# Kernel tuning notes

Measured on AMD Instinct MI355X. Metric: run time of the kernel, lower is better.

## Reference

```python
import jax, jax.numpy as jnp
import numpy as np
import math

L = 8           # n_layers
DIM = 1024
H = 16          # num_heads
HD = DIM // H   # head_dim
HID = 4096      # mlp hidden
V = 32000       # vocab
B, T = 2, 1024


def setup_inputs() -> dict:
    key = jax.random.key(0)
    ks = jax.random.split(key, 10)
    s = 0.02
    inp = {
        "input_ids": jax.random.randint(ks[0], (B, T), 0, V, dtype=jnp.int32),
        "labels": jax.random.randint(ks[1], (B, T), 0, V, dtype=jnp.int32),
        "Wemb": jax.random.normal(ks[2], (V, DIM), jnp.float32) * s,   # tied embed / lm_head
        "Wq": jax.random.normal(ks[3], (L, DIM, DIM), jnp.float32) * s,
        "Wk": jax.random.normal(ks[4], (L, DIM, DIM), jnp.float32) * s,
        "Wv": jax.random.normal(ks[5], (L, DIM, DIM), jnp.float32) * s,
        "Wo": jax.random.normal(ks[6], (L, DIM, DIM), jnp.float32) * s,
        "Wfc": jax.random.normal(ks[7], (L, DIM, HID), jnp.float32) * s,
        "Wgate": jax.random.normal(ks[8], (L, DIM, HID), jnp.float32) * s,
        "Wproj": jax.random.normal(ks[9], (L, HID, DIM), jnp.float32) * s,
    }
    return inp


def _forward(input_ids, labels, Wemb, Wq, Wk, Wv, Wo, Wfc, Wgate, Wproj):
    b, t = input_ids.shape
    h = Wemb[input_ids]                                   # [B,T,C] embedding lookup
    # causal additive mask: -inf strictly above diagonal
    mask = jnp.triu(jnp.full((t, t), -jnp.inf, dtype=h.dtype), k=1)
    inv_sqrt_L = 1.0 / math.sqrt(L)
    inv_sqrt_hd = 1.0 / math.sqrt(HD)
    inv_sqrt_hid = 1.0 / math.sqrt(HID)

    def block(h, params):
        wq, wk, wv, wo, wfc, wgate, wproj = params
        # attention (explicit QK^T softmax V, as in source)
        q = (h @ wq).reshape(b, t, H, HD)
        k = (h @ wk).reshape(b, t, H, HD)
        v = (h @ wv).reshape(b, t, H, HD)
        scores = jnp.einsum("bqhd,bkhd->bhqk", q, k) * inv_sqrt_hd + mask
        probs = jax.nn.softmax(scores, axis=-1)
        attn = jnp.einsum("bhqk,bkhd->bqhd", probs, v).reshape(b, t, DIM)
        h = h + (attn @ wo) * inv_sqrt_L
        # SwiGLU MLP with 1/sqrt(hidden) scaling
        mlp = (((h @ wfc) * jax.nn.silu(h @ wgate)) * inv_sqrt_hid) @ wproj
        h = h + mlp * inv_sqrt_L
        return h, None

    h, _ = jax.lax.scan(block, h, (Wq, Wk, Wv, Wo, Wfc, Wgate, Wproj))

    logits = h @ Wemb.T                                   # tied lm_head [B,T,V]
    # cross entropy with ignore_index=-1
    lab = labels.reshape(-1)
    valid = lab != -1
    safe = jnp.where(valid, lab, 0)
    logp = jax.nn.log_softmax(logits.reshape(-1, V), axis=-1)
    nll = -jnp.take_along_axis(logp, safe[:, None], axis=-1)[:, 0]
    loss = jnp.sum(jnp.where(valid, nll, 0.0)) / jnp.maximum(jnp.sum(valid), 1)
    return logits, loss


def reference(input_ids, labels, Wemb, Wq, Wk, Wv, Wo, Wfc, Wgate, Wproj):
    return _forward(input_ids, labels, Wemb, Wq, Wk, Wv, Wo, Wfc, Wgate, Wproj)
```

## Files before the change

### kernel.cpp

```cpp
#include <hip/hip_runtime.h>
#include <hip/hip_bf16.h>
#include <math.h>

#define L_LAYERS 8
#define DIM 1024
#define NH 16
#define HD 64
#define HID 4096
#define VOCAB 32000
#define BB 2
#define TT 1024
#define MROWS (BB*TT)

typedef unsigned short u16;
typedef short short8 __attribute__((ext_vector_type(8)));
typedef float f32x4 __attribute__((ext_vector_type(4)));
typedef unsigned short us4 __attribute__((ext_vector_type(4)));
typedef unsigned short us8 __attribute__((ext_vector_type(8)));

__device__ __forceinline__ float bf2f(u16 x){
  union { unsigned int u; float f; } v; v.u = ((unsigned int)x) << 16; return v.f;
}
__device__ __forceinline__ u16 f2bf(float f){
  union { float f; unsigned int u; } v; v.f = f;
  unsigned int r = (v.u + 0x7fffu + ((v.u >> 16) & 1u)) >> 16; return (u16)r;
}

#define AS1 __attribute__((address_space(1)))
#define AS3 __attribute__((address_space(3)))
__device__ __forceinline__ void gld_lds16(const void* g, void* l){
  __builtin_amdgcn_global_load_lds((const AS1 void*)g, (AS3 void*)l, 16, 0, 0);
}

__global__ void k_embed(const int* __restrict__ ids, const float* __restrict__ Wemb,
                        float* __restrict__ h, u16* __restrict__ hb){
  int bt = blockIdx.x; long id = ids[bt];
  const float4* src = (const float4*)(Wemb + id*(long)DIM);
  float4 v = src[threadIdx.x];
  ((float4*)(h + (long)bt*DIM))[threadIdx.x] = v;
  us4 o = { f2bf(v.x), f2bf(v.y), f2bf(v.z), f2bf(v.w) };
  ((us4*)(hb + (long)bt*DIM))[threadIdx.x] = o;
}

__global__ void k_cvt(const float* __restrict__ src, u16* __restrict__ dst, long n){
  long i = ((long)blockIdx.x*256 + threadIdx.x)*8;
  if (i >= n) return;
  float4 a = ((const float4*)(src+i))[0];
  float4 b = ((const float4*)(src+i))[1];
  us4 o0 = { f2bf(a.x), f2bf(a.y), f2bf(a.z), f2bf(a.w) };
  us4 o1 = { f2bf(b.x), f2bf(b.y), f2bf(b.z), f2bf(b.w) };
  ((us4*)(dst+i))[0] = o0; ((us4*)(dst+i))[1] = o1;
}

__global__ void k_cvt_layer(const float* __restrict__ Wq, const float* __restrict__ Wk,
    const float* __restrict__ Wv, const float* __restrict__ Wo,
    const float* __restrict__ Wfc, const float* __restrict__ Wg, const float* __restrict__ Wp,
    u16* __restrict__ qkvT, u16* __restrict__ woT, u16* __restrict__ fgT, u16* __restrict__ projT)
{
  int tile = blockIdx.x;
  const float* src; u16* dst; int R, C, tr, tc;
  long rowmul = 1, rowoff = 0;
  if (tile < 1024){
    int m = tile >> 8, t2 = tile & 255;
    tr = t2 >> 4; tc = t2 & 15; R = 1024; C = 1024;
    src = (m==0)?Wq:(m==1)?Wk:(m==2)?Wv:Wo;
    dst = (m<3)? qkvT + (long)m*1024*1024 : woT;
  } else if (tile < 3072){
    int m = (tile - 1024) >> 10, t2 = (tile - 1024) & 1023;
    tr = t2 >> 6; tc = t2 & 63; R = 1024; C = 4096;
    src = m ? Wg : Wfc; dst = fgT; rowmul = 2; rowoff = m;
  } else {
    int t2 = tile - 3072;
    tr = t2 >> 4; tc = t2 & 15; R = 4096; C = 1024;
    src = Wp; dst = projT;
  }
  __shared__ float ls[64][65];
  int u = threadIdx.x, rr = u & 63, cc = u >> 6;
  const float* sp = src + (long)(tr*64 + rr)*C + tc*64 + cc*16;
  float4 v0 = ((const float4*)sp)[0];
  float4 v1 = ((const float4*)sp)[1];
  float4 v2 = ((const float4*)sp)[2];
  float4 v3 = ((const float4*)sp)[3];
  ls[rr][cc*16+ 0]=v0.x; ls[rr][cc*16+ 1]=v0.y; ls[rr][cc*16+ 2]=v0.z; ls[rr][cc*16+ 3]=v0.w;
  ls[rr][cc*16+ 4]=v1.x; ls[rr][cc*16+ 5]=v1.y; ls[rr][cc*16+ 6]=v1.z; ls[rr][cc*16+ 7]=v1.w;
  ls[rr][cc*16+ 8]=v2.x; ls[rr][cc*16+ 9]=v2.y; ls[rr][cc*16+10]=v2.z; ls[rr][cc*16+11]=v2.w;
  ls[rr][cc*16+12]=v3.x; ls[rr][cc*16+13]=v3.y; ls[rr][cc*16+14]=v3.z; ls[rr][cc*16+15]=v3.w;
  __syncthreads();
  int d  = u >> 2;
  int c4 = u & 3;
  long drow = (long)tc*64 + d;
  u16* dp = dst + (drow*rowmul + rowoff)*R + tr*64;
  #pragma unroll
  for (int g2 = 0; g2 < 2; ++g2){
    int e0 = (c4 + g2*4) * 8;
    us8 o;
    #pragma unroll
    for (int j=0;j<8;j++) o[j] = f2bf(ls[e0+j][d]);
    *((us8*)(dp + e0)) = o;
  }
}

template<int EPI>
__global__ __launch_bounds__(256, 2) void k_gemm(
    const u16* __restrict__ A, long lda,
    const u16* __restrict__ Bt, long ldb,
    void* __restrict__ Cp, long ldc,
    int K, int nMt, float alpha, int ksplit,
    u16* __restrict__ hbout)
{
  __shared__ u16 lsA[128*32];
  __shared__ u16 lsB[128*32];
  int nflat = gridDim.x; int w = blockIdx.x;
  if ((nflat & 7) == 0){ int q = nflat >> 3; w = (w & 7)*q + (w >> 3); }
  int perk = nflat / ksplit;
  int kc = w / perk; int w2 = w - kc*perk;
  int mtile = w2 % nMt, ntile = w2 / nMt;
  const u16* Ab = A + (long)mtile*128*lda + (long)kc*K;
  const u16* Bb = Bt + (long)ntile*128*ldb + (long)kc*K;
  int t = threadIdx.x;
  int wv = t >> 6, ln = t & 63;
  int srow = t >> 2;
  int scol = (t & 3) * 8;
  int fr = ln & 15, kg = ln >> 4;
  int wr = wv >> 1, wc = wv & 1;
  const f32x4 zero = {0.f,0.f,0.f,0.f};
  f32x4 acc[4][4];
  #pragma unroll
  for (int m=0;m<4;m++)
    #pragma unroll
    for (int n=0;n<4;n++) acc[m][n] = zero;
  const u16* ga0 = Ab + (long)srow*lda + scol;
  const u16* ga1 = Ab + (long)(srow+64)*lda + scol;
  const u16* gb0 = Bb + (long)srow*ldb + scol;
  const u16* gb1 = Bb + (long)(srow+64)*ldb + scol;
  u16* la0 = lsA + wv*512;
  u16* la1 = lsA + 2048 + wv*512;
  u16* lb0 = lsB + wv*512;
  u16* lb1 = lsB + 2048 + wv*512;
  for (int k0 = 0; k0 < K; k0 += 32){
    gld_lds16(ga0 + k0, la0);
    gld_lds16(ga1 + k0, la1);
    gld_lds16(gb0 + k0, lb0);
    gld_lds16(gb1 + k0, lb1);
    __syncthreads();
    short8 af[4], bfr[4];
    #pragma unroll
    for (int m=0;m<4;m++) af[m]  = *(const short8*)(lsA + (wr*64 + m*16 + fr)*32 + kg*8);
    #pragma unroll
    for (int n=0;n<4;n++) bfr[n] = *(const short8*)(lsB + (wc*64 + n*16 + fr)*32 + kg*8);
    #pragma unroll
    for (int m=0;m<4;m++)
      #pragma unroll
      for (int n=0;n<4;n++)
        acc[m][n] = __builtin_amdgcn_mfma_f32_16x16x32_bf16(af[m], bfr[n], acc[m][n], 0, 0, 0);
    __syncthreads();
  }
  long row0 = (long)mtile*128 + wr*64 + kg*4;
  int col0 = ntile*128 + wc*64 + fr;
  if constexpr (EPI == 0){
    u16* C = (u16*)Cp;
    #pragma unroll
    for (int m=0;m<4;m++)
      #pragma unroll
      for (int r=0;r<4;r++){
        long row = row0 + m*16 + r;
        #pragma unroll
        for (int n=0;n<4;n++) C[row*ldc + col0 + n*16] = f2bf(acc[m][n][r]);
      }
  } else if constexpr (EPI == 2){
    float* C = (float*)Cp;
    #pragma unroll
    for (int m=0;m<4;m++)
      #pragma unroll
      for (int r=0;r<4;r++){
        long row = row0 + m*16 + r;
        #pragma unroll
        for (int n=0;n<4;n++){
          long idx = row*ldc + col0 + n*16;
          float v = C[idx] + acc[m][n][r]*alpha;
          C[idx] = v;
          hbout[idx] = f2bf(v);
        }
      }
  } else {
    float* C = (float*)Cp + (long)kc*MROWS*ldc;
    #pragma unroll
    for (int m=0;m<4;m++)
      #pragma unroll
      for (int r=0;r<4;r++){
        long row = row0 + m*16 + r;
        #pragma unroll
        for (int n=0;n<4;n++) C[row*ldc + col0 + n*16] = acc[m][n][r];
      }
  }
}

__global__ void k_redK(const float* __restrict__ pK, float* __restrict__ h, u16* __restrict__ hb){
  long idx = ((long)blockIdx.x*256 + threadIdx.x)*4;
  const float aL = 0.35355339059327373f;
  float4 s0 = *(const float4*)(pK + idx);
  float4 s1 = *(const float4*)(pK + idx + (long)MROWS*1024);
  float4 s2 = *(const float4*)(pK + idx + (long)2*MROWS*1024);
  float4 s3 = *(const float4*)(pK + idx + (long)3*MROWS*1024);
  float4 hv = *(const float4*)(h + idx);
  float4 v;
  v.x = hv.x + (s0.x+s1.x+s2.x+s3.x)*aL;
  v.y = hv.y + (s0.y+s1.y+s2.y+s3.y)*aL;
  v.z = hv.z + (s0.z+s1.z+s2.z+s3.z)*aL;
  v.w = hv.w + (s0.w+s1.w+s2.w+s3.w)*aL;
  *(float4*)(h + idx) = v;
  us4 o = { f2bf(v.x), f2bf(v.y), f2bf(v.z), f2bf(v.w) };
  *(us4*)(hb + idx) = o;
}

#define RD256(base, row, ku) (*(const short8*)((base) + (row)*64 + ((((ku) ^ ((row)&7)))<<3)))

template<int EPI>
__global__ __launch_bounds__(512, 1) void k_gemm256(
    const u16* __restrict__ A, long lda,
    const u16* __restrict__ Bt, long ldb,
    void* __restrict__ Cp, long ldc,
    int K, int nMt,
    float2* __restrict__ partials)
{
  __shared__ u16 lds[65536];
  int nwg = gridDim.x; int w = blockIdx.x;
  { int q = nwg >> 3, r8 = nwg & 7; int xcd = w & 7, lw = w >> 3;
    w = (xcd < r8 ? xcd*(q+1) : r8*(q+1) + (xcd-r8)*q) + lw; }
  int mtile = w % nMt, ntile = w / nMt;
  const u16* Abase = A + (long)mtile*256*lda;
  const u16* Bbase = Bt + (long)ntile*256*ldb;
  int tid = threadIdx.x;
  int wid = tid >> 6, ln = tid & 63;
  int wm = wid >> 2, wn = wid & 3;
  int fr = ln & 15, kg = ln >> 4;

  f32x4 acc[8][4];
  #pragma unroll
  for (int a=0;a<8;a++)
    #pragma unroll
    for (int b=0;b<4;b++) acc[a][b] = (f32x4){0.f,0.f,0.f,0.f};

#define STAGE_A(i, kofs, dstbase) do{ \
    int u_ = (i)*512 + tid; int r_ = u_>>3; int cu_ = u_&7; \
    gld_lds16(Abase + (long)r_*lda + (kofs) + ((cu_^(r_&7))<<3), \
              (dstbase) + (((i)*512 + wid*64)<<3)); }while(0)
#define STAGE_B(i, kofs, dstbase) do{ \
    int u_ = (i)*512 + tid; int r_ = u_>>3; int cu_ = u_&7; \
    gld_lds16(Bbase + (long)r_*ldb + (kofs) + ((cu_^(r_&7))<<3), \
              (dstbase) + (((i)*512 + wid*64)<<3)); }while(0)

#define QUADK(mh, nh, ks) do{ \
    short8 a0 = RD256(ldsA, wm*128 + (mh)*64 +  0 + fr, (ks)*4+kg); \
    short8 a1 = RD256(ldsA, wm*128 + (mh)*64 + 16 + fr, (ks)*4+kg); \
    short8 a2 = RD256(ldsA, wm*128 + (mh)*64 + 32 + fr, (ks)*4+kg); \
    short8 a3 = RD256(ldsA, wm*128 + (mh)*64 + 48 + fr, (ks)*4+kg); \
    short8 b0 = RD256(ldsB, wn*64 + (nh)*32 +  0 + fr, (ks)*4+kg); \
    short8 b1 = RD256(ldsB, wn*64 + (nh)*32 + 16 + fr, (ks)*4+kg); \
    acc[(mh)*4+0][(nh)*2+0] = __builtin_amdgcn_mfma_f32_16x16x32_bf16(a0,b0,acc[(mh)*4+0][(nh)*2+0],0,0,0); \
    acc[(mh)*4+1][(nh)*2+0] = __builtin_amdgcn_mfma_f32_16x16x32_bf16(a1,b0,acc[(mh)*4+1][(nh)*2+0],0,0,0); \
    acc[(mh)*4+2][(nh)*2+0] = __builtin_amdgcn_mfma_f32_16x16x32_bf16(a2,b0,acc[(mh)*4+2][(nh)*2+0],0,0,0); \
    acc[(mh)*4+3][(nh)*2+0] = __builtin_amdgcn_mfma_f32_16x16x32_bf16(a3,b0,acc[(mh)*4+3][(nh)*2+0],0,0,0); \
    acc[(mh)*4+0][(nh)*2+1] = __builtin_amdgcn_mfma_f32_16x16x32_bf16(a0,b1,acc[(mh)*4+0][(nh)*2+1],0,0,0); \
    acc[(mh)*4+1][(nh)*2+1] = __builtin_amdgcn_mfma_f32_16x16x32_bf16(a1,b1,acc[(mh)*4+1][(nh)*2+1],0,0,0); \
    acc[(mh)*4+2][(nh)*2+1] = __builtin_amdgcn_mfma_f32_16x16x32_bf16(a2,b1,acc[(mh)*4+2][(nh)*2+1],0,0,0); \
    acc[(mh)*4+3][(nh)*2+1] = __builtin_amdgcn_mfma_f32_16x16x32_bf16(a3,b1,acc[(mh)*4+3][(nh)*2+1],0,0,0); \
  }while(0)

  {
    u16* dA = lds; u16* dB = lds + 16384;
    STAGE_A(0, 0, dA); STAGE_A(1, 0, dA); STAGE_A(2, 0, dA); STAGE_A(3, 0, dA);
    STAGE_B(0, 0, dB); STAGE_B(1, 0, dB); STAGE_B(2, 0, dB); STAGE_B(3, 0, dB);
  }
  const int NT = K >> 6;
  #pragma unroll 2
  for (int jt = 0; jt < NT; ++jt){
    int bsel = jt & 1;
    u16* ldsA = lds + bsel*32768;
    u16* ldsB = ldsA + 16384;
    u16* nA = lds + (bsel^1)*32768;
    u16* nB = nA + 16384;
    long k1 = (long)(jt+1) << 6;
    bool pref = (jt+1 < NT);
    if (pref){
      STAGE_A(0, k1, nA); STAGE_A(1, k1, nA);
      STAGE_B(0, k1, nB); STAGE_B(1, k1, nB);
      asm volatile("s_waitcnt vmcnt(4)" ::: "memory");
    } else {
      asm volatile("s_waitcnt vmcnt(0)" ::: "memory");
    }
    __builtin_amdgcn_s_barrier();
    __builtin_amdgcn_s_setprio(1);
    QUADK(0,0,0); QUADK(0,0,1);
    QUADK(0,1,0); QUADK(0,1,1);
    __builtin_amdgcn_s_setprio(0);
    __builtin_amdgcn_sched_barrier(0);
    if (pref){
      STAGE_A(2, k1, nA); STAGE_A(3, k1, nA);
      STAGE_B(2, k1, nB); STAGE_B(3, k1, nB);
    }
    __builtin_amdgcn_sched_barrier(0);
    __builtin_amdgcn_s_setprio(1);
    QUADK(1,0,0); QUADK(1,0,1);
    QUADK(1,1,0); QUADK(1,1,1);
    __builtin_amdgcn_s_setprio(0);
    __builtin_amdgcn_sched_barrier(0);
    __builtin_amdgcn_s_barrier();
  }

  if constexpr (EPI == 3){
    u16* act = (u16*)Cp;
    const float sc = 0.015625f;
    #pragma unroll
    for (int a=0;a<8;a++)
      #pragma unroll
      for (int r=0;r<4;r++){
        long row = (long)mtile*256 + wm*128 + a*16 + kg*4 + r;
        #pragma unroll
        for (int b=0;b<4;b++){
          float v = acc[a][b][r];
          float pv = __shfl_xor(v, 1);
          if (!(fr & 1)){
            int colg = ntile*256 + wn*64 + (b>>1)*32 + (b&1)*16 + fr;
            float g = pv;
            float sl = g / (1.0f + __expf(-g));
            act[row*ldc + (colg>>1)] = f2bf(v * sl * sc);
          }
        }
      }
  } else {
    float* C = (float*)Cp;
    #pragma unroll
    for (int a=0;a<8;a++)
      #pragma unroll
      for (int r=0;r<4;r++){
        long row = (long)mtile*256 + wm*128 + a*16 + kg*4 + r;
        #pragma unroll
        for (int b=0;b<4;b++){
          int colg = ntile*256 + wn*64 + (b>>1)*32 + (b&1)*16 + fr;
          C[row*ldc + colg] = acc[a][b][r];
        }
      }
    float* pm = (float*)lds;
    float* ps = pm + 1024;
    #pragma unroll
    for (int a=0;a<8;a++)
      #pragma unroll
      for (int r=0;r<4;r++){
        float M = fmaxf(fmaxf(acc[a][0][r],acc[a][1][r]), fmaxf(acc[a][2][r],acc[a][3][r]));
        #pragma unroll
        for (int o=1;o<16;o<<=1) M = fmaxf(M, __shfl_xor(M, o));
        float S = __expf(acc[a][0][r]-M) + __expf(acc[a][1][r]-M)
                + __expf(acc[a][2][r]-M) + __expf(acc[a][3][r]-M);
        #pragma unroll
        for (int o=1;o<16;o<<=1) S += __shfl_xor(S, o);
        if (fr == 0){
          int rl = wm*128 + a*16 + kg*4 + r;
          pm[wn*256 + rl] = M; ps[wn*256 + rl] = S;
        }
      }
    __syncthreads();
    if (tid < 256){
      float m0 = pm[tid], m1 = pm[256+tid], m2 = pm[512+tid], m3 = pm[768+tid];
      float M = fmaxf(fmaxf(m0,m1), fmaxf(m2,m3));
      float S = ps[tid]*__expf(m0-M) + ps[256+tid]*__expf(m1-M)
              + ps[512+tid]*__expf(m2-M) + ps[768+tid]*__expf(m3-M);
      partials[((long)mtile*256 + tid)*128 + ntile] = make_float2(M, S);
    }
  }
#undef STAGE_A
#undef STAGE_B
#undef QUADK
}

__global__ void k_transpose_v(const u16* __restrict__ qkv, u16* __restrict__ vT){
  int ttile = blockIdx.x; int z = blockIdx.y;
  long b = z >> 4; int hh = z & 15;
  const u16* v = qkv + b*TT*3072 + 2048 + hh*64;
  u16* outp = vT + (long)z*64*TT;
  __shared__ u16 ls[64][65];
  int u = threadIdx.x, rr = u & 63, cc = u >> 6;
  const u16* sp = v + (long)(ttile*64 + rr)*3072 + cc*16;
  us4 a0 = ((const us4*)sp)[0];
  us4 a1 = ((const us4*)sp)[1];
  us4 a2 = ((const us4*)sp)[2];
  us4 a3 = ((const us4*)sp)[3];
  #pragma unroll
  for (int j=0;j<4;j++){ ls[rr][cc*16+j] = a0[j]; ls[rr][cc*16+4+j] = a1[j];
                         ls[rr][cc*16+8+j] = a2[j]; ls[rr][cc*16+12+j] = a3[j]; }
  __syncthreads();
  int d = u & 63;
  #pragma unroll
  for (int g=0; g<4; ++g){
    int tl = cc*16 + g*4;
    int t  = ttile*64 + tl;
    int ut = (t >> 3) & 15;
    int tp = (t & ~127) + (((ut ^ (d & 15)) << 3) | (t & 7));
    us4 o = { ls[tl+0][d], ls[tl+1][d], ls[tl+2][d], ls[tl+3][d] };
    *((us4*)(outp + (long)d*TT + tp)) = o;
  }
}

__global__ __launch_bounds__(128) void k_flash(
    const u16* __restrict__ qkv, const u16* __restrict__ vT, u16* __restrict__ attnb)
{
  __shared__ u16 lsQ[64*64];
  __shared__ u16 lsK[128*64];
  __shared__ u16 lsV[64*128];
  __shared__ u16 lsP[64*128];
  int qt = blockIdx.x; int z = blockIdx.y;
  long bT = (long)(z >> 4) * TT;
  int h64 = (z & 15) * 64;
  int t = threadIdx.x, wv = t >> 6, ln = t & 63;
  int fr = ln & 15, kg = ln >> 4;
  const u16* vbase = vT + (long)z*64*TT;

  #pragma unroll
  for (int p=0; p<4; ++p){
    int r = p*16 + wv*8 + (ln>>3);
    const u16* g = qkv + (bT + qt*64 + r)*3072 + h64 + (((ln&7) ^ (ln>>3))*8);
    gld_lds16(g, lsQ + (p*16 + wv*8)*64);
  }

  f32x4 S[2][8], O[2][4];
  float Mst[2][4], Lst[2][4];
  #pragma unroll
  for (int m=0;m<2;m++){
    #pragma unroll
    for (int n=0;n<4;n++) O[m][n] = (f32x4){0.f,0.f,0.f,0.f};
    #pragma unroll
    for (int r=0;r<4;r++){ Mst[m][r] = -3.0e38f; Lst[m][r] = 0.f; }
  }

  int nk = (qt >> 1) + 1;
  for (int kt = 0; kt < nk; ++kt){
    #pragma unroll
    for (int p=0; p<8; ++p){
      int r = p*16 + wv*8 + (ln>>3);
      const u16* g = qkv + (bT + kt*128 + r)*3072 + 1024 + h64 + (((ln&7) ^ (ln>>3))*8);
      gld_lds16(g, lsK + (p*16 + wv*8)*64);
    }
    #pragma unroll
    for (int p=0; p<8; ++p){
      int d = p*8 + wv*4 + (ln>>4);
      const u16* g = vbase + (long)d*TT + kt*128 + (ln&15)*8;
      gld_lds16(g, lsV + (p*8 + wv*4)*128);
    }
    __syncthreads();

    #pragma unroll
    for (int m=0;m<2;m++)
      #pragma unroll
      for (int n=0;n<8;n++) S[m][n] = (f32x4){0.f,0.f,0.f,0.f};
    #pragma unroll
    for (int ks=0; ks<2; ++ks){
      int un = ((ks*4 + kg) ^ (fr & 7)) * 8;
      short8 a0 = *(const short8*)(lsQ + (wv*32 +      fr)*64 + un);
      short8 a1 = *(const short8*)(lsQ + (wv*32 + 16 + fr)*64 + un);
      #pragma unroll
      for (int n=0;n<8;n++){
        short8 bb = *(const short8*)(lsK + (n*16 + fr)*64 + un);
        S[0][n] = __builtin_amdgcn_mfma_f32_16x16x32_bf16(a0, bb, S[0][n], 0,0,0);
        S[1][n] = __builtin_amdgcn_mfma_f32_16x16x32_bf16(a1, bb, S[1][n], 0,0,0);
      }
    }

    #pragma unroll
    for (int m=0;m<2;m++){
      #pragma unroll
      for (int r=0;r<4;r++){
        int rloc = wv*32 + m*16 + kg*4 + r;
        int row_g = qt*64 + rloc;
        float x[8]; float mx = -3.0e38f;
        #pragma unroll
        for (int n=0;n<8;n++){
          int col_g = kt*128 + n*16 + fr;
          x[n] = (col_g <= row_g) ? S[m][n][r]*0.125f : -3.0e38f;
          mx = fmaxf(mx, x[n]);
        }
        #pragma unroll
        for (int o=1;o<16;o<<=1) mx = fmaxf(mx, __shfl_xor(mx, o));
        float Mnew = fmaxf(Mst[m][r], mx);
        float corr = __expf(Mst[m][r] - Mnew);
        Mst[m][r] = Mnew;
        float s = 0.f;
        #pragma unroll
        for (int n=0;n<8;n++){
          float p = __expf(x[n] - Mnew);
          s += p;
          int col = n*16 + fr;
          int col2 = ((((col>>3) ^ (rloc & 15)) << 3) | (col & 7));
          lsP[rloc*128 + col2] = f2bf(p);
        }
        #pragma unroll
        for (int o=1;o<16;o<<=1) s += __shfl_xor(s, o);
        Lst[m][r] = Lst[m][r]*corr + s;
        #pragma unroll
        for (int n=0;n<4;n++) O[m][n][r] *= corr;
      }
    }

    #pragma unroll
    for (int ks=0; ks<4; ++ks){
      int up = ((ks*4 + kg) ^ fr) * 8;
      short8 p0 = *(const short8*)(lsP + (wv*32 +      fr)*128 + up);
      short8 p1 = *(const short8*)(lsP + (wv*32 + 16 + fr)*128 + up);
      #pragma unroll
      for (int n=0;n<4;n++){
        short8 vb = *(const short8*)(lsV + (n*16 + fr)*128 + up);
        O[0][n] = __builtin_amdgcn_mfma_f32_16x16x32_bf16(p0, vb, O[0][n], 0,0,0);
        O[1][n] = __builtin_amdgcn_mfma_f32_16x16x32_bf16(p1, vb, O[1][n], 0,0,0);
      }
    }
    __syncthreads();
  }

  #pragma unroll
  for (int m=0;m<2;m++)
    #pragma unroll
    for (int r=0;r<4;r++){
      float inv = 1.0f / Lst[m][r];
      long row = bT + qt*64 + wv*32 + m*16 + kg*4 + r;
      #pragma unroll
      for (int n=0;n<4;n++)
        attnb[row*1024 + h64 + n*16 + fr] = f2bf(O[m][n][r]*inv);
    }
}

__global__ void k_nll2(const float2* __restrict__ part, const float* __restrict__ logits,
                       const int* __restrict__ labels, float* __restrict__ nll){
  int row = blockIdx.x; int ln = threadIdx.x;
  const float2* pr = part + (long)row*128;
  float m = -3.0e38f, s = 0.f;
  for (int j = ln; j < 125; j += 64){
    float2 p = pr[j];
    float M = fmaxf(m, p.x);
    s = s*__expf(m - M) + p.y*__expf(p.x - M);
    m = M;
  }
  #pragma unroll
  for (int o=32;o;o>>=1){
    float om = __shfl_xor(m, o), os = __shfl_xor(s, o);
    float M = fmaxf(m, om);
    s = s*__expf(m - M) + os*__expf(om - M);
    m = M;
  }
  if (ln == 0){
    int lab = labels[row];
    float lse = m + __logf(s);
    nll[row] = (lab != -1) ? (lse - logits[(long)row*VOCAB + lab]) : 0.f;
  }
}

__global__ void k_loss(const float* __restrict__ nll, const int* __restrict__ labels,
                       float* __restrict__ out){
  int tid = threadIdx.x;
  int wv = tid >> 6;
  float s = 0.f; float c = 0.f;
  for (int i = tid; i < MROWS; i += 256){
    s += nll[i];
    c += (labels[i] != -1) ? 1.f : 0.f;
  }
  #pragma unroll
  for (int o=32;o;o>>=1){ s += __shfl_xor(s, o); c += __shfl_xor(c, o); }
  __shared__ float rsm[4], rc[4];
  if ((tid & 63) == 0){ rsm[wv] = s; rc[wv] = c; }
  __syncthreads();
  if (tid == 0){
    s = rsm[0]+rsm[1]+rsm[2]+rsm[3];
    c = rc[0]+rc[1]+rc[2]+rc[3];
    out[(long)MROWS*VOCAB] = s / fmaxf(c, 1.f);
  }
}

extern "C" void kernel_launch(void* const* d_in, const int* in_sizes, int n_in,
                              void* d_out, int out_size, void* d_ws, size_t ws_size,
                              hipStream_t stream)
{
  (void)in_sizes; (void)n_in; (void)out_size; (void)ws_size;
  const int*   ids    = (const int*)d_in[0];
  const int*   labels = (const int*)d_in[1];
  const float* Wemb   = (const float*)d_in[2];
  const float* Wq     = (const float*)d_in[3];
  const float* Wk     = (const float*)d_in[4];
  const float* Wv     = (const float*)d_in[5];
  const float* Wo     = (const float*)d_in[6];
  const float* Wfc    = (const float*)d_in[7];
  const float* Wg     = (const float*)d_in[8];
  const float* Wp     = (const float*)d_in[9];
  float* logits = (float*)d_out;

  char* ws = (char*)d_ws;
  size_t off = 0;
  auto alloc = [&](size_t bytes){ void* p = ws + off; off += (bytes + 255) & ~(size_t)255; return p; };
  u16*    wembBf = (u16*)alloc((size_t)VOCAB*DIM*2);
  float*  h      = (float*)alloc((size_t)MROWS*DIM*4);
  u16*    hb     = (u16*)alloc((size_t)MROWS*DIM*2);
  u16*    qkvT   = (u16*)alloc((size_t)3*DIM*DIM*2);
  u16*    woT    = (u16*)alloc((size_t)DIM*DIM*2);
  u16*    fgT    = (u16*)alloc((size_t)2*HID*DIM*2);
  u16*    projT  = (u16*)alloc((size_t)DIM*HID*2);
  u16*    qkv    = (u16*)alloc((size_t)MROWS*3*DIM*2);
  u16*    vT     = (u16*)alloc((size_t)BB*NH*64*TT*2);
  u16*    attnb  = (u16*)alloc((size_t)MROWS*DIM*2);
  u16*    act    = (u16*)alloc((size_t)MROWS*HID*2);
  float*  pK     = (float*)alloc((size_t)4*MROWS*DIM*4);
  float2* parts  = (float2*)alloc((size_t)MROWS*128*8);
  float*  nllb   = (float*)alloc((size_t)MROWS*4);

  dim3 blk(256,1,1);
  dim3 blk512(512,1,1);
  const float aL = 0.35355339059327373f;

  k_cvt<<<dim3(16000,1,1),blk,0,stream>>>(Wemb, wembBf, (long)VOCAB*DIM);
  k_embed<<<dim3(MROWS,1,1),blk,0,stream>>>(ids, Wemb, h, hb);

  for (int l = 0; l < L_LAYERS; ++l){
    k_cvt_layer<<<dim3(4096,1,1),blk,0,stream>>>(
        Wq + (size_t)l*DIM*DIM, Wk + (size_t)l*DIM*DIM, Wv + (size_t)l*DIM*DIM, Wo + (size_t)l*DIM*DIM,
        Wfc + (size_t)l*DIM*HID, Wg + (size_t)l*DIM*HID, Wp + (size_t)l*HID*DIM,
        qkvT, woT, fgT, projT);
    k_gemm<0><<<dim3(384,1,1),blk,0,stream>>>(hb,1024, qkvT,1024, qkv,3072,
        1024,16,1.f,1, nullptr);
    k_transpose_v<<<dim3(16,32,1),blk,0,stream>>>(qkv, vT);
    k_flash<<<dim3(16,32,1),dim3(128,1,1),0,stream>>>(qkv, vT, attnb);
    k_gemm<2><<<dim3(128,1,1),blk,0,stream>>>(attnb,1024, woT,1024, h,1024,
        1024,16,aL,1, hb);
    k_gemm256<3><<<dim3(256,1,1),blk512,0,stream>>>(hb,1024, fgT,1024, act,4096,
        1024,8, nullptr);
    k_gemm<5><<<dim3(512,1,1),blk,0,stream>>>(act,4096, projT,4096, pK,1024,
        1024,16,1.f,4, nullptr);
    k_redK<<<dim3(2048,1,1),blk,0,stream>>>(pK, h, hb);
  }
  k_gemm256<4><<<dim3(1000,1,1),blk512,0,stream>>>(hb,1024, wembBf,1024, logits,32000,
      1024,8, parts);
  k_nll2<<<dim3(MROWS,1,1),dim3(64,1,1),0,stream>>>(parts, logits, labels, nllb);
  k_loss<<<dim3(1,1,1),blk,0,stream>>>(nllb, labels, logits);
}
```

Measured before the change: 1.913 ms.

## Restructure 256x256 GEMM main loop into 8-slot half-tile ping-pong pipeline

Rewrites the k_gemm256 main loop to split A and B tiles into 128-row halves held in eight LDS slots. Each of four phases per K-step issues its LDS reads, then one half-tile global prefetch, then a barrier and 16 MFMAs, so loads are spread evenly across the compute. Warp tiling changes from a contiguous 128x64 block per wave to interleaved 64x32 sub-blocks in each half, and the epilogue row and column mapping is updated to match. The aim is finer-grained overlap of global-to-LDS loads with MFMA work, at the cost of more barriers per K-step and more complex slot bookkeeping.

```diff
diff --git a/kernel.cpp b/kernel.cpp
--- a/kernel.cpp
+++ b/kernel.cpp
@@ -213,7 +213,55 @@
   *(us4*)(hb + idx) = o;
 }
 
-#define RD256(base, row, ku) (*(const short8*)((base) + (row)*64 + ((((ku) ^ ((row)&7)))<<3)))
+#define MFMA_(va,vb,vc) __builtin_amdgcn_mfma_f32_16x16x32_bf16(va,vb,vc,0,0,0)
+#define RD(slot, row, ku) (*(const short8*)(lds + (slot)*8192 + (row)*64 + ((((ku) ^ ((row)&7)))<<3)))
+#define STG(base, ld, h, k0, slot) do{ \
+    int u0_ = tid, r0_ = u0_>>3, c0_ = u0_&7; \
+    gld_lds16((base) + (long)((h)*128 + r0_)*(ld) + (k0) + ((c0_^(r0_&7))<<3), \
+              lds + (slot)*8192 + (wid*64)*8); \
+    int u1_ = 512 + tid, r1_ = u1_>>3, c1_ = u1_&7; \
+    gld_lds16((base) + (long)((h)*128 + r1_)*(ld) + (k0) + ((c1_^(r1_&7))<<3), \
+              lds + (slot)*8192 + (512 + wid*64)*8); \
+  }while(0)
+#define PHASE(sA, sB, mh, nh, SC, SBASE, SLD, SH, SKOFS, SSLOT, DOWAIT) do{ \
+    short8 a00 = RD(sA, wm*64 +  0 + fr, kg); \
+    short8 a01 = RD(sA, wm*64 + 16 + fr, kg); \
+    short8 a02 = RD(sA, wm*64 + 32 + fr, kg); \
+    short8 a03 = RD(sA, wm*64 + 48 + fr, kg); \
+    short8 a10 = RD(sA, wm*64 +  0 + fr, 4+kg); \
+    short8 a11 = RD(sA, wm*64 + 16 + fr, 4+kg); \
+    short8 a12 = RD(sA, wm*64 + 32 + fr, 4+kg); \
+    short8 a13 = RD(sA, wm*64 + 48 + fr, 4+kg); \
+    short8 b00 = RD(sB, wn*32 +  0 + fr, kg); \
+    short8 b01 = RD(sB, wn*32 + 16 + fr, kg); \
+    short8 b10 = RD(sB, wn*32 +  0 + fr, 4+kg); \
+    short8 b11 = RD(sB, wn*32 + 16 + fr, 4+kg); \
+    if (SC) STG(SBASE, SLD, SH, SKOFS, SSLOT); \
+    if (DOWAIT){ \
+      if (SC) asm volatile("s_waitcnt vmcnt(4)" ::: "memory"); \
+      else    asm volatile("s_waitcnt vmcnt(0)" ::: "memory"); \
+    } \
+    asm volatile("s_barrier" ::: "memory"); \
+    __builtin_amdgcn_s_setprio(1); \
+    acc[(mh)*4+0][(nh)*2+0] = MFMA_(a00,b00,acc[(mh)*4+0][(nh)*2+0]); \
+    acc[(mh)*4+1][(nh)*2+0] = MFMA_(a01,b00,acc[(mh)*4+1][(nh)*2+0]); \
+    acc[(mh)*4+2][(nh)*2+0] = MFMA_(a02,b00,acc[(mh)*4+2][(nh)*2+0]); \
+    acc[(mh)*4+3][(nh)*2+0] = MFMA_(a03,b00,acc[(mh)*4+3][(nh)*2+0]); \
+    acc[(mh)*4+0][(nh)*2+1] = MFMA_(a00,b01,acc[(mh)*4+0][(nh)*2+1]); \
+    acc[(mh)*4+1][(nh)*2+1] = MFMA_(a01,b01,acc[(mh)*4+1][(nh)*2+1]); \
+    acc[(mh)*4+2][(nh)*2+1] = MFMA_(a02,b01,acc[(mh)*4+2][(nh)*2+1]); \
+    acc[(mh)*4+3][(nh)*2+1] = MFMA_(a03,b01,acc[(mh)*4+3][(nh)*2+1]); \
+    acc[(mh)*4+0][(nh)*2+0] = MFMA_(a10,b10,acc[(mh)*4+0][(nh)*2+0]); \
+    acc[(mh)*4+1][(nh)*2+0] = MFMA_(a11,b10,acc[(mh)*4+1][(nh)*2+0]); \
+    acc[(mh)*4+2][(nh)*2+0] = MFMA_(a12,b10,acc[(mh)*4+2][(nh)*2+0]); \
+    acc[(mh)*4+3][(nh)*2+0] = MFMA_(a13,b10,acc[(mh)*4+3][(nh)*2+0]); \
+    acc[(mh)*4+0][(nh)*2+1] = MFMA_(a10,b11,acc[(mh)*4+0][(nh)*2+1]); \
+    acc[(mh)*4+1][(nh)*2+1] = MFMA_(a11,b11,acc[(mh)*4+1][(nh)*2+1]); \
+    acc[(mh)*4+2][(nh)*2+1] = MFMA_(a12,b11,acc[(mh)*4+2][(nh)*2+1]); \
+    acc[(mh)*4+3][(nh)*2+1] = MFMA_(a13,b11,acc[(mh)*4+3][(nh)*2+1]); \
+    __builtin_amdgcn_s_setprio(0); \
+    asm volatile("s_barrier" ::: "memory"); \
+  }while(0)
 
 template<int EPI>
 __global__ __launch_bounds__(512, 1) void k_gemm256(
@@ -241,106 +289,74 @@
     #pragma unroll
     for (int b=0;b<4;b++) acc[a][b] = (f32x4){0.f,0.f,0.f,0.f};
 
-#define STAGE_A(i, kofs, dstbase) do{ \
-    int u_ = (i)*512 + tid; int r_ = u_>>3; int cu_ = u_&7; \
-    gld_lds16(Abase + (long)r_*lda + (kofs) + ((cu_^(r_&7))<<3), \
-              (dstbase) + (((i)*512 + wid*64)<<3)); }while(0)
-#define STAGE_B(i, kofs, dstbase) do{ \
-    int u_ = (i)*512 + tid; int r_ = u_>>3; int cu_ = u_&7; \
-    gld_lds16(Bbase + (long)r_*ldb + (kofs) + ((cu_^(r_&7))<<3), \
-              (dstbase) + (((i)*512 + wid*64)<<3)); }while(0)
-
-#define QUADK(mh, nh, ks) do{ \
-    short8 a0 = RD256(ldsA, wm*128 + (mh)*64 +  0 + fr, (ks)*4+kg); \
-    short8 a1 = RD256(ldsA, wm*128 + (mh)*64 + 16 + fr, (ks)*4+kg); \
-    short8 a2 = RD256(ldsA, wm*128 + (mh)*64 + 32 + fr, (ks)*4+kg); \
-    short8 a3 = RD256(ldsA, wm*128 + (mh)*64 + 48 + fr, (ks)*4+kg); \
-    short8 b0 = RD256(ldsB, wn*64 + (nh)*32 +  0 + fr, (ks)*4+kg); \
-    short8 b1 = RD256(ldsB, wn*64 + (nh)*32 + 16 + fr, (ks)*4+kg); \
-    acc[(mh)*4+0][(nh)*2+0] = __builtin_amdgcn_mfma_f32_16x16x32_bf16(a0,b0,acc[(mh)*4+0][(nh)*2+0],0,0,0); \
-    acc[(mh)*4+1][(nh)*2+0] = __builtin_amdgcn_mfma_f32_16x16x32_bf16(a1,b0,acc[(mh)*4+1][(nh)*2+0],0,0,0); \
-    acc[(mh)*4+2][(nh)*2+0] = __builtin_amdgcn_mfma_f32_16x16x32_bf16(a2,b0,acc[(mh)*4+2][(nh)*2+0],0,0,0); \
-    acc[(mh)*4+3][(nh)*2+0] = __builtin_amdgcn_mfma_f32_16x16x32_bf16(a3,b0,acc[(mh)*4+3][(nh)*2+0],0,0,0); \
-    acc[(mh)*4+0][(nh)*2+1] = __builtin_amdgcn_mfma_f32_16x16x32_bf16(a0,b1,acc[(mh)*4+0][(nh)*2+1],0,0,0); \
-    acc[(mh)*4+1][(nh)*2+1] = __builtin_amdgcn_mfma_f32_16x16x32_bf16(a1,b1,acc[(mh)*4+1][(nh)*2+1],0,0,0); \
-    acc[(mh)*4+2][(nh)*2+1] = __builtin_amdgcn_mfma_f32_16x16x32_bf16(a2,b1,acc[(mh)*4+2][(nh)*2+1],0,0,0); \
-    acc[(mh)*4+3][(nh)*2+1] = __builtin_amdgcn_mfma_f32_16x16x32_bf16(a3,b1,acc[(mh)*4+3][(nh)*2+1],0,0,0); \
-  }while(0)
-
-  {
-    u16* dA = lds; u16* dB = lds + 16384;
-    STAGE_A(0, 0, dA); STAGE_A(1, 0, dA); STAGE_A(2, 0, dA); STAGE_A(3, 0, dA);
-    STAGE_B(0, 0, dB); STAGE_B(1, 0, dB); STAGE_B(2, 0, dB); STAGE_B(3, 0, dB);
-  }
   const int NT = K >> 6;
-  #pragma unroll 2
-  for (int jt = 0; jt < NT; ++jt){
-    int bsel = jt & 1;
-    u16* ldsA = lds + bsel*32768;
-    u16* ldsB = ldsA + 16384;
-    u16* nA = lds + (bsel^1)*32768;
-    u16* nB = nA + 16384;
-    long k1 = (long)(jt+1) << 6;
-    bool pref = (jt+1 < NT);
-    if (pref){
-      STAGE_A(0, k1, nA); STAGE_A(1, k1, nA);
-      STAGE_B(0, k1, nB); STAGE_B(1, k1, nB);
-      asm volatile("s_waitcnt vmcnt(4)" ::: "memory");
-    } else {
-      asm volatile("s_waitcnt vmcnt(0)" ::: "memory");
-    }
-    __builtin_amdgcn_s_barrier();
-    __builtin_amdgcn_s_setprio(1);
-    QUADK(0,0,0); QUADK(0,0,1);
-    QUADK(0,1,0); QUADK(0,1,1);
-    __builtin_amdgcn_s_setprio(0);
-    __builtin_amdgcn_sched_barrier(0);
-    if (pref){
-      STAGE_A(2, k1, nA); STAGE_A(3, k1, nA);
-      STAGE_B(2, k1, nB); STAGE_B(3, k1, nB);
-    }
-    __builtin_amdgcn_sched_barrier(0);
-    __builtin_amdgcn_s_setprio(1);
-    QUADK(1,0,0); QUADK(1,0,1);
-    QUADK(1,1,0); QUADK(1,1,1);
-    __builtin_amdgcn_s_setprio(0);
-    __builtin_amdgcn_sched_barrier(0);
-    __builtin_amdgcn_s_barrier();
+  STG(Abase, lda, 0, 0, 0);
+  STG(Bbase, ldb, 0, 0, 2);
+  STG(Abase, lda, 1, 0, 1);
+  STG(Bbase, ldb, 1, 0, 3);
+  if (NT > 1){
+    STG(Abase, lda, 0, 64, 4);
+    STG(Bbase, ldb, 1, 64, 7);
+    asm volatile("s_waitcnt vmcnt(4)" ::: "memory");
+  } else {
+    asm volatile("s_waitcnt vmcnt(0)" ::: "memory");
+  }
+  asm volatile("s_barrier" ::: "memory");
+
+  for (int jt = 0; jt < NT; jt += 2){
+    {
+      long k1 = ((long)jt+1)<<6, k2 = ((long)jt+2)<<6;
+      bool s1 = (jt+1 < NT), s2 = (jt+2 < NT);
+      PHASE(0,2,0,0, s1, Abase, lda, 1, k1, 5, 0);
+      PHASE(0,3,0,1, s1, Bbase, ldb, 0, k1, 6, 0);
+      PHASE(1,3,1,1, s2, Abase, lda, 0, k2, 0, 0);
+      PHASE(1,2,1,0, s2, Bbase, ldb, 1, k2, 3, 1);
+    }
+    if (jt+1 < NT){
+      long k1 = ((long)jt+2)<<6, k2 = ((long)jt+3)<<6;
+      bool s1 = (jt+2 < NT), s2 = (jt+3 < NT);
+      PHASE(4,6,0,0, s1, Abase, lda, 1, k1, 1, 0);
+      PHASE(4,7,0,1, s1, Bbase, ldb, 0, k1, 2, 0);
+      PHASE(5,7,1,1, s2, Abase, lda, 0, k2, 4, 0);
+      PHASE(5,6,1,0, s2, Bbase, ldb, 1, k2, 7, 1);
+    }
   }
 
   if constexpr (EPI == 3){
     u16* act = (u16*)Cp;
     const float sc = 0.015625f;
     #pragma unroll
-    for (int a=0;a<8;a++)
+    for (int a=0;a<8;a++){
+      long rowb = (long)mtile*256 + (a>>2)*128 + wm*64 + (a&3)*16 + kg*4;
       #pragma unroll
       for (int r=0;r<4;r++){
-        long row = (long)mtile*256 + wm*128 + a*16 + kg*4 + r;
         #pragma unroll
         for (int b=0;b<4;b++){
           float v = acc[a][b][r];
           float pv = __shfl_xor(v, 1);
           if (!(fr & 1)){
-            int colg = ntile*256 + wn*64 + (b>>1)*32 + (b&1)*16 + fr;
+            int colg = ntile*256 + (b>>1)*128 + wn*32 + (b&1)*16 + fr;
             float g = pv;
             float sl = g / (1.0f + __expf(-g));
-            act[row*ldc + (colg>>1)] = f2bf(v * sl * sc);
+            act[(rowb+r)*ldc + (colg>>1)] = f2bf(v * sl * sc);
           }
         }
       }
+    }
   } else {
     float* C = (float*)Cp;
     #pragma unroll
-    for (int a=0;a<8;a++)
+    for (int a=0;a<8;a++){
+      long rowb = (long)mtile*256 + (a>>2)*128 + wm*64 + (a&3)*16 + kg*4;
       #pragma unroll
       for (int r=0;r<4;r++){
-        long row = (long)mtile*256 + wm*128 + a*16 + kg*4 + r;
         #pragma unroll
         for (int b=0;b<4;b++){
-          int colg = ntile*256 + wn*64 + (b>>1)*32 + (b&1)*16 + fr;
-          C[row*ldc + colg] = acc[a][b][r];
+          int colg = ntile*256 + (b>>1)*128 + wn*32 + (b&1)*16 + fr;
+          C[(rowb+r)*ldc + colg] = acc[a][b][r];
         }
       }
+    }
     float* pm = (float*)lds;
     float* ps = pm + 1024;
     #pragma unroll
@@ -355,7 +371,7 @@
         #pragma unroll
         for (int o=1;o<16;o<<=1) S += __shfl_xor(S, o);
         if (fr == 0){
-          int rl = wm*128 + a*16 + kg*4 + r;
+          int rl = (a>>2)*128 + wm*64 + (a&3)*16 + kg*4 + r;
           pm[wn*256 + rl] = M; ps[wn*256 + rl] = S;
         }
       }
@@ -368,9 +384,6 @@
       partials[((long)mtile*256 + tid)*128 + ntile] = make_float2(M, S);
     }
   }
-#undef STAGE_A
-#undef STAGE_B
-#undef QUADK
 }
 
 __global__ void k_transpose_v(const u16* __restrict__ qkv, u16* __restrict__ vT){
```

Measured after the change: 1.973 ms. +3.2%, slower.
